# Kernel tuning notes

Hardware: AMD Instinct MI355X
Metric: run time of the kernel (lower is better)

## Reference

```python
import jax, jax.numpy as jnp
import numpy as np

N, E, B, H = 100000, 1600000, 16, 128
LN_EPS = 1e-5


def _ln(x, g, b):
    mu = jnp.mean(x, axis=-1, keepdims=True)
    v = jnp.mean(jnp.square(x - mu), axis=-1, keepdims=True)
    return (x - mu) * jax.lax.rsqrt(v + LN_EPS) * g + b


def setup_inputs() -> dict:
    key = jax.random.key(0)
    ks = iter(jax.random.split(key, 48))
    rn = lambda shape, s=0.05: jax.random.normal(next(ks), shape, jnp.float32) * s
    inp = {}
    inp['x'] = jax.random.normal(next(ks), (N, 3), jnp.float32)
    inp['edge_attr'] = jax.random.normal(next(ks), (E, 3), jnp.float32)
    inp['edge_index'] = jax.random.randint(next(ks), (2, E), 0, N, dtype=jnp.int32)
    inp['batch'] = jnp.sort(jax.random.randint(next(ks), (N,), 0, B, dtype=jnp.int32))
    # node encoder
    inp['ne_w1'] = rn((3, H)); inp['ne_b1'] = jnp.zeros((H,), jnp.float32)
    inp['ne_w2'] = rn((H, H)); inp['ne_b2'] = jnp.zeros((H,), jnp.float32)
    inp['ne_g'] = jnp.ones((H,), jnp.float32); inp['ne_be'] = jnp.zeros((H,), jnp.float32)
    # edge encoder
    inp['ee_w1'] = rn((3, H)); inp['ee_b1'] = jnp.zeros((H,), jnp.float32)
    inp['ee_w2'] = rn((H, H)); inp['ee_b2'] = jnp.zeros((H,), jnp.float32)
    inp['ee_g'] = jnp.ones((H,), jnp.float32); inp['ee_be'] = jnp.zeros((H,), jnp.float32)
    # GINEConv layers (stacked over num_layers=2)
    L = 2
    inp['gin_eps'] = jnp.zeros((L,), jnp.float32)
    inp['gin_w1'] = rn((L, H, H)); inp['gin_b1'] = jnp.zeros((L, H), jnp.float32)
    inp['gin_w2'] = rn((L, H, H)); inp['gin_b2'] = jnp.zeros((L, H), jnp.float32)
    inp['gin_g'] = jnp.ones((L, H), jnp.float32); inp['gin_be'] = jnp.zeros((L, H), jnp.float32)
    # global processor
    inp['gp_w'] = rn((H, H)); inp['gp_b'] = jnp.zeros((H,), jnp.float32)
    inp['gp_g'] = jnp.ones((H,), jnp.float32); inp['gp_be'] = jnp.zeros((H,), jnp.float32)
    # edge predictor
    inp['ep_w1'] = rn((4 * H, 2 * H)); inp['ep_b1'] = jnp.zeros((2 * H,), jnp.float32)
    inp['ep_w2'] = rn((2 * H, H)); inp['ep_b2'] = jnp.zeros((H,), jnp.float32)
    inp['ep_w3'] = rn((H, 1)); inp['ep_b3'] = jnp.zeros((1,), jnp.float32)
    return inp


def _forward(x, edge_attr, edge_index, batch,
             ne_w1, ne_b1, ne_w2, ne_b2, ne_g, ne_be,
             ee_w1, ee_b1, ee_w2, ee_b2, ee_g, ee_be,
             gin_eps, gin_w1, gin_b1, gin_w2, gin_b2, gin_g, gin_be,
             gp_w, gp_b, gp_g, gp_be,
             ep_w1, ep_b1, ep_w2, ep_b2, ep_w3, ep_b3):
    src, dst = edge_index[0], edge_index[1]
    # node / edge encoders (dropout = identity in eval mode)
    h = _ln(jax.nn.relu(x @ ne_w1 + ne_b1) @ ne_w2 + ne_b2, ne_g, ne_be)          # [N,H]
    e = _ln(jax.nn.relu(edge_attr @ ee_w1 + ee_b1) @ ee_w2 + ee_b2, ee_g, ee_be)  # [E,H]
    num_layers = gin_eps.shape[0]
    for l in range(num_layers):
        # GINE: out = MLP((1+eps)*x + sum_j relu(x_j + e_ij))
        msg = jax.nn.relu(h[src] + e)                                    # [E,H]
        agg = jax.ops.segment_sum(msg, dst, num_segments=N)              # [N,H]
        z = (1.0 + gin_eps[l]) * h + agg
        h = _ln(jax.nn.relu(z @ gin_w1[l] + gin_b1[l]) @ gin_w2[l] + gin_b2[l], gin_g[l], gin_be[l])
        if l < num_layers - 1:
            h = jax.nn.relu(h)
    # global mean pool over graphs
    gsum = jax.ops.segment_sum(h, batch, num_segments=B)                 # [B,H]
    cnt = jax.ops.segment_sum(jnp.ones((h.shape[0], 1), h.dtype), batch, num_segments=B)
    g = gsum / jnp.maximum(cnt, 1.0)
    g = _ln(jax.nn.relu(g @ gp_w + gp_b), gp_g, gp_be)                   # [B,H]
    # per-edge scores
    comb = jnp.concatenate([h[src], h[dst], g[batch[src]], e], axis=-1)  # [E,4H]
    s = jnp.tanh(comb @ ep_w1 + ep_b1)
    s = jnp.tanh(s @ ep_w2 + ep_b2)
    return jax.nn.sigmoid(s @ ep_w3 + ep_b3)                             # [E,1]


def reference(x, edge_attr, edge_index, batch,
              ne_w1, ne_b1, ne_w2, ne_b2, ne_g, ne_be,
              ee_w1, ee_b1, ee_w2, ee_b2, ee_g, ee_be,
              gin_eps, gin_w1, gin_b1, gin_w2, gin_b2, gin_g, gin_be,
              gp_w, gp_b, gp_g, gp_be,
              ep_w1, ep_b1, ep_w2, ep_b2, ep_w3, ep_b3):
    return _forward(x, edge_attr, edge_index, batch,
                    ne_w1, ne_b1, ne_w2, ne_b2, ne_g, ne_be,
                    ee_w1, ee_b1, ee_w2, ee_b2, ee_g, ee_be,
                    gin_eps, gin_w1, gin_b1, gin_w2, gin_b2, gin_g, gin_be,
                    gp_w, gp_b, gp_g, gp_be,
                    ep_w1, ep_b1, ep_w2, ep_b2, ep_w3, ep_b3)
```

## Files before the change

### kernel.cpp

```cpp
#include <hip/hip_runtime.h>
#include <stdint.h>

typedef unsigned short u16;
typedef short bf16x8 __attribute__((ext_vector_type(8)));
typedef float f32x4 __attribute__((ext_vector_type(4)));

#define DEV __device__ __forceinline__

DEV float bf2f(u16 u){ union{uint32_t i; float f;} v; v.i = ((uint32_t)u)<<16; return v.f; }
DEV u16 f2bf(float f){ union{float f; uint32_t i;} v; v.f=f; uint32_t u=v.i; u += 0x7FFFu + ((u>>16)&1u); return (u16)(u>>16); }
DEV uint32_t cvt_pk_bf16(float lo, float hi){
    uint32_t r;
    asm("v_cvt_pk_bf16_f32 %0, %1, %2" : "=v"(r) : "v"(lo), "v"(hi));
    return r;
}
DEV bf16x8 pack8(const float* v){
    union { bf16x8 b; uint32_t u[4]; } o;
    #pragma unroll
    for (int k=0;k<4;k++) o.u[k] = cvt_pk_bf16(v[2*k], v[2*k+1]);
    return o.b;
}
DEV float fast_tanh(float x){ float t=__builtin_amdgcn_exp2f(x*2.885390081777927f); return 1.f-2.f*__builtin_amdgcn_rcpf(t+1.f); }
DEV float fast_sigmoid(float x){ return __builtin_amdgcn_rcpf(1.f+__builtin_amdgcn_exp2f(-1.4426950408889634f*x)); }
DEV f32x4 mfma16(bf16x8 a, bf16x8 b, f32x4 c){ return __builtin_amdgcn_mfma_f32_16x16x32_bf16(a,b,c,0,0,0); }
DEV void atomAddF(float* p, float v){ __hip_atomic_fetch_add(p, v, __ATOMIC_RELAXED, __HIP_MEMORY_SCOPE_AGENT); }
DEV void barrier_lds(){
    asm volatile("s_waitcnt lgkmcnt(0)" ::: "memory");
    __builtin_amdgcn_s_barrier();
    __builtin_amdgcn_sched_barrier(0);
}

__global__ void diag_kernel(float* out, float v){ if (threadIdx.x < 8) out[threadIdx.x] = v; }

__global__ __launch_bounds__(256) void prep_all(
    const float* __restrict__ ne_w2, const float* __restrict__ ee_w2,
    const float* __restrict__ gin_w1, const float* __restrict__ gin_w2,
    const float* __restrict__ ep_w1, const float* __restrict__ ep_w2,
    u16* __restrict__ ne_w2T, u16* __restrict__ ee_w2T,
    u16* __restrict__ gw1T0, u16* __restrict__ gw1T1,
    u16* __restrict__ gw2T0, u16* __restrict__ gw2T1,
    u16* __restrict__ w1aT, u16* __restrict__ w1bT,
    u16* __restrict__ w1dT, u16* __restrict__ epw2T)
{
    int b = blockIdx.x, tid = threadIdx.x;
    const float* src; u16* dst; int ld, K, Nn, base;
    if      (b < 64)  { src=ne_w2;          dst=ne_w2T; ld=128; K=128; Nn=128; base=0;   }
    else if (b < 128) { src=ee_w2;          dst=ee_w2T; ld=128; K=128; Nn=128; base=64;  }
    else if (b < 192) { src=gin_w1;         dst=gw1T0;  ld=128; K=128; Nn=128; base=128; }
    else if (b < 256) { src=gin_w1+128*128; dst=gw1T1;  ld=128; K=128; Nn=128; base=192; }
    else if (b < 320) { src=gin_w2;         dst=gw2T0;  ld=128; K=128; Nn=128; base=256; }
    else if (b < 384) { src=gin_w2+128*128; dst=gw2T1;  ld=128; K=128; Nn=128; base=320; }
    else if (b < 512) { src=ep_w1;          dst=w1aT;   ld=256; K=128; Nn=256; base=384; }
    else if (b < 640) { src=ep_w1+128*256;  dst=w1bT;   ld=256; K=128; Nn=256; base=512; }
    else if (b < 768) { src=ep_w1+384*256;  dst=w1dT;   ld=256; K=128; Nn=256; base=640; }
    else              { src=ep_w2;          dst=epw2T;  ld=128; K=256; Nn=128; base=768; }
    int idx = (b-base)*256 + tid;
    if (idx >= K*Nn) return;
    int n = idx / K, k = idx - n*K;
    dst[(n*K + k) ^ ((n&7)<<3)] = f2bf(src[(size_t)k*ld + n]);
}

__global__ __launch_bounds__(256) void hist_kernel(const int* __restrict__ dst,
                                                   int* __restrict__ deg, int E)
{
    int e = blockIdx.x*256 + threadIdx.x;
    if (e < E) atomicAdd(&deg[dst[e]], 1);
}

__global__ __launch_bounds__(1024) void scan_kernel(const int* __restrict__ deg,
                                                    int* __restrict__ cur, int N)
{
    __shared__ int sc[1024];
    int t = threadIdx.x;
    int chunk = (N + 1023) / 1024;
    int i0 = t * chunk, i1 = i0 + chunk; if (i1 > N) i1 = N;
    int s = 0;
    for (int i = i0; i < i1; i++) s += deg[i];
    sc[t] = s; __syncthreads();
    int own = s;
    for (int off = 1; off < 1024; off <<= 1){
        int v = (t >= off) ? sc[t - off] : 0;
        __syncthreads();
        sc[t] += v;
        __syncthreads();
    }
    int run = sc[t] - own;
    for (int i = i0; i < i1; i++){ cur[i] = run; run += deg[i]; }
}

__global__ __launch_bounds__(256) void scatter_kernel(
    const int* __restrict__ src, const int* __restrict__ dst, const float* __restrict__ ea,
    int* __restrict__ cur, int* __restrict__ src_s, int* __restrict__ dst_s,
    float* __restrict__ ea_s, int E)
{
    int e = blockIdx.x*256 + threadIdx.x;
    if (e >= E) return;
    int d = dst[e];
    int pos = atomicAdd(&cur[d], 1);
    src_s[pos] = src[e];
    dst_s[pos] = d;
    ea_s[(size_t)pos*3+0] = ea[(size_t)e*3+0];
    ea_s[(size_t)pos*3+1] = ea[(size_t)e*3+1];
    ea_s[(size_t)pos*3+2] = ea[(size_t)e*3+2];
}

__global__ __launch_bounds__(256) void enc_kernel(
    const float* __restrict__ in3, int rows,
    const float* __restrict__ w1, const float* __restrict__ b1,
    const u16* __restrict__ w2T, const float* __restrict__ b2,
    const float* __restrict__ gam, const float* __restrict__ bet,
    float* __restrict__ outF)
{
    __shared__ u16 wbs[128*128];
    __shared__ u16 hid[64*128];
    int tid = threadIdx.x, r0 = blockIdx.x*64;
    for (int i = tid; i < 8192; i += 256) ((uint32_t*)wbs)[i] = ((const uint32_t*)w2T)[i];
    for (int idx = tid; idx < 8192; idx += 256) {
        int r = idx >> 7, c = idx & 127;
        int row = r0 + r; if (row > rows-1) row = rows-1;
        float v = b1[c] + in3[(size_t)row*3+0]*w1[c] + in3[(size_t)row*3+1]*w1[128+c] + in3[(size_t)row*3+2]*w1[256+c];
        hid[idx ^ ((r&7)<<3)] = f2bf(fmaxf(v, 0.f));
    }
    barrier_lds();
    int lane = tid & 63, w = tid >> 6, l16 = lane & 15, q = lane >> 4;
    int ar = 16*w + l16;
    f32x4 acc[8];
    #pragma unroll
    for (int nt=0; nt<8; nt++) acc[nt] = (f32x4){0.f,0.f,0.f,0.f};
    #pragma unroll
    for (int ks=0; ks<4; ks++) {
        bf16x8 af = *(const bf16x8*)&hid[(ar*128 + ks*32 + q*8) ^ ((ar&7)<<3)];
        #pragma unroll
        for (int nt=0; nt<8; nt++) {
            int n = nt*16 + l16;
            bf16x8 bfr = *(const bf16x8*)&wbs[(n*128 + ks*32 + q*8) ^ ((n&7)<<3)];
            acc[nt] = mfma16(af, bfr, acc[nt]);
        }
    }
    float b2v[8], gv[8], bv[8];
    #pragma unroll
    for (int nt=0; nt<8; nt++){ int c = nt*16+l16; b2v[nt]=b2[c]; gv[nt]=gam[c]; bv[nt]=bet[c]; }
    #pragma unroll
    for (int reg=0; reg<4; reg++) {
        float s=0.f, ss=0.f;
        #pragma unroll
        for (int nt=0; nt<8; nt++){ float v = acc[nt][reg] + b2v[nt]; acc[nt][reg]=v; s+=v; ss+=v*v; }
        #pragma unroll
        for (int m=1; m<16; m<<=1){ s += __shfl_xor(s,m); ss += __shfl_xor(ss,m); }
        float mean = s * (1.f/128.f);
        float rstd = __builtin_amdgcn_rsqf(ss*(1.f/128.f) - mean*mean + 1e-5f);
        int row = r0 + 16*w + 4*q + reg;
        if (row < rows) {
            #pragma unroll
            for (int nt=0; nt<8; nt++){
                int c = nt*16+l16;
                outF[(size_t)row*128 + c] = (acc[nt][reg]-mean)*rstd*gv[nt] + bv[nt];
            }
        }
    }
}

__global__ __launch_bounds__(256) void msg_v3(
    const float* __restrict__ ea_s, const int* __restrict__ src_s, const int* __restrict__ dst_s,
    const float* __restrict__ ew1, const float* __restrict__ eb1,
    const u16* __restrict__ ew2T, const float* __restrict__ eb2,
    const float* __restrict__ eg, const float* __restrict__ ebe,
    const float* __restrict__ h, float* __restrict__ agg, int E)
{
    __shared__ float lag[8192];
    __shared__ u16 hid[64*128];
    __shared__ float eas[192];
    __shared__ float w1s[384];
    __shared__ float b1s[128];
    __shared__ int ssrc[64], sdv[64], sslot[64], sfl[64];
    u16* wbs = (u16*)lag;
    int tid = threadIdx.x, r0 = blockIdx.x*64;

    const uint4* w4 = (const uint4*)ew2T;
    uint4 pr[8];
    #pragma unroll
    for (int k=0;k<8;k++) pr[k] = w4[tid + k*256];

    if (tid < 192){ int gi = r0*3 + tid; eas[tid] = (gi < E*3) ? ea_s[gi] : 0.f; }
    if (tid < 128) b1s[tid] = eb1[tid];
    for (int i = tid; i < 384; i += 256) w1s[i] = ew1[i];
    if (tid < 64){
        int r = tid, ge = r0 + r;
        int valid = ge < E;
        int gc = valid ? ge : E-1;
        int dv = dst_s[gc];
        int sv = src_s[gc];
        int pin = __shfl_up(dv, 1);
        int head = (r == 0) || (dv != pin);
        int prevLast  = (r0 > 0)      ? dst_s[r0-1]  : -2;
        int nextFirst = (r0 + 64 < E) ? dst_s[r0+64] : -2;
        int interior = (dv != prevLast) && (dv != nextFirst);
        int s = head ? r : 0;
        #pragma unroll
        for (int off=1; off<64; off<<=1){ int v = __shfl_up(s, off); if (r >= off) s = (s > v ? s : v); }
        ssrc[r]=sv; sdv[r]=dv; sslot[r]=s;
        sfl[r] = ((head && valid)?1:0) | (interior?2:0) | (valid?4:0);
    }
    barrier_lds();
    int g = tid >> 5, cgm = (tid & 31) << 2;
    float4 hv[8];
    #pragma unroll
    for (int k=0;k<8;k++)
        hv[k] = *(const float4*)(h + (size_t)ssrc[g*8+k]*128 + cgm);
    {
        uint4* wb4 = (uint4*)wbs;
        #pragma unroll
        for (int k=0;k<8;k++) wb4[tid + k*256] = pr[k];
    }
    barrier_lds();

    int lane = tid&63, w = tid>>6, l16 = lane&15, q = lane>>4;
    int ar = 16*w + l16;
    float ea0 = eas[ar*3], ea1 = eas[ar*3+1], ea2 = eas[ar*3+2];
    f32x4 acc[8];
    #pragma unroll
    for (int nt=0; nt<8; nt++) acc[nt] = (f32x4){0.f,0.f,0.f,0.f};
    #pragma unroll
    for (int ks=0; ks<4; ks++){
        float hv8[8];
        #pragma unroll
        for (int j=0;j<8;j++){
            int c = ks*32 + q*8 + j;
            hv8[j] = fmaxf(b1s[c] + ea0*w1s[c] + ea1*w1s[128+c] + ea2*w1s[256+c], 0.f);
        }
        bf16x8 ah = pack8(hv8);
        #pragma unroll
        for (int nt=0; nt<8; nt++){
            int n = nt*16 + l16;
            bf16x8 bfr = *(const bf16x8*)&wbs[(n*128 + ks*32 + q*8) ^ ((n&7)<<3)];
            acc[nt] = mfma16(ah, bfr, acc[nt]);
        }
    }
    {
        float b2v[8], gv[8], bv[8];
        #pragma unroll
        for (int nt=0; nt<8; nt++){ int c = nt*16+l16; b2v[nt]=eb2[c]; gv[nt]=eg[c]; bv[nt]=ebe[c]; }
        #pragma unroll
        for (int reg=0; reg<4; reg++){
            float s=0.f, ss=0.f;
            #pragma unroll
            for (int nt=0; nt<8; nt++){ float v = acc[nt][reg] + b2v[nt]; acc[nt][reg]=v; s+=v; ss+=v*v; }
            #pragma unroll
            for (int m=1; m<16; m<<=1){ s += __shfl_xor(s,m); ss += __shfl_xor(ss,m); }
            float mean = s*(1.f/128.f);
            float rstd = __builtin_amdgcn_rsqf(ss*(1.f/128.f)-mean*mean+1e-5f);
            int rl = 16*w + 4*q + reg;
            #pragma unroll
            for (int nt=0; nt<8; nt+=2){
                float v0 = (acc[nt][reg]-mean)*rstd*gv[nt] + bv[nt];
                float v1 = (acc[nt+1][reg]-mean)*rstd*gv[nt+1] + bv[nt+1];
                uint32_t pk = cvt_pk_bf16(v0, v1);
                hid[rl*128 + nt*16 + l16]     = (u16)pk;
                hid[rl*128 + (nt+1)*16 + l16] = (u16)(pk >> 16);
            }
        }
    }
    barrier_lds();
    for (int i = tid; i < 8192; i += 256) lag[i] = 0.f;
    barrier_lds();

    {
        float4 a = {0.f,0.f,0.f,0.f};
        int cur = -1;
        #pragma unroll
        for (int k=0;k<8;k++){
            int r = g*8 + k;
            if (sfl[r] & 4){
                uint2 ev = *(const uint2*)&hid[r*128 + cgm];
                float4 m;
                m.x = fmaxf(hv[k].x + bf2f((u16)(ev.x & 0xFFFF)), 0.f);
                m.y = fmaxf(hv[k].y + bf2f((u16)(ev.x >> 16)),   0.f);
                m.z = fmaxf(hv[k].z + bf2f((u16)(ev.y & 0xFFFF)), 0.f);
                m.w = fmaxf(hv[k].w + bf2f((u16)(ev.y >> 16)),   0.f);
                int slot = sslot[r];
                if (slot != cur){
                    if (cur >= 0){
                        float* lp = lag + cur*128 + cgm;
                        atomicAdd(lp+0,a.x); atomicAdd(lp+1,a.y); atomicAdd(lp+2,a.z); atomicAdd(lp+3,a.w);
                    }
                    cur = slot; a = m;
                } else {
                    a.x += m.x; a.y += m.y; a.z += m.z; a.w += m.w;
                }
            }
        }
        if (cur >= 0){
            float* lp = lag + cur*128 + cgm;
            atomicAdd(lp+0,a.x); atomicAdd(lp+1,a.y); atomicAdd(lp+2,a.z); atomicAdd(lp+3,a.w);
        }
    }
    barrier_lds();
    for (int t = tid; t < 2048; t += 256){
        int r = t >> 5, cg = (t & 31) << 2;
        int fl = sfl[r];
        if (!(fl & 1)) continue;
        float4 v = *(const float4*)&lag[r*128 + cg];
        float* gp = agg + (size_t)sdv[r]*128 + cg;
        if (fl & 2){ *(float4*)gp = v; }
        else { atomAddF(gp+0,v.x); atomAddF(gp+1,v.y); atomAddF(gp+2,v.z); atomAddF(gp+3,v.w); }
    }
}

__global__ __launch_bounds__(256) void gine_update(
    float* h, const float* __restrict__ agg,
    const float* __restrict__ epsArr, int layer,
    const u16* __restrict__ w1T, const u16* __restrict__ w2T,
    const float* __restrict__ b1, const float* __restrict__ b2,
    const float* __restrict__ gam, const float* __restrict__ bet,
    int rows, int doRelu)
{
    __shared__ u16 wbs[128*128];
    __shared__ u16 hid[64*128];
    int tid = threadIdx.x, r0 = blockIdx.x*64;
    float epsv = 1.f + epsArr[layer];
    for (int i = tid; i < 8192; i += 256) ((uint32_t*)wbs)[i] = ((const uint32_t*)w1T)[i];
    barrier_lds();
    int lane = tid&63, w = tid>>6, l16 = lane&15, q = lane>>4;
    int ar = 16*w + l16;
    int arow = r0 + ar;
    int arc = arow < rows ? arow : rows-1;
    f32x4 acc[8];
    #pragma unroll
    for (int nt=0; nt<8; nt++) acc[nt] = (f32x4){0.f,0.f,0.f,0.f};
    #pragma unroll
    for (int ks=0; ks<4; ks++){
        const float4* hp = (const float4*)(h   + (size_t)arc*128 + ks*32 + q*8);
        const float4* ap = (const float4*)(agg + (size_t)arc*128 + ks*32 + q*8);
        float4 h0 = hp[0], h1 = hp[1], a0 = ap[0], a1 = ap[1];
        float zv[8];
        zv[0]=fmaf(epsv,h0.x,a0.x); zv[1]=fmaf(epsv,h0.y,a0.y);
        zv[2]=fmaf(epsv,h0.z,a0.z); zv[3]=fmaf(epsv,h0.w,a0.w);
        zv[4]=fmaf(epsv,h1.x,a1.x); zv[5]=fmaf(epsv,h1.y,a1.y);
        zv[6]=fmaf(epsv,h1.z,a1.z); zv[7]=fmaf(epsv,h1.w,a1.w);
        bf16x8 af = pack8(zv);
        #pragma unroll
        for (int nt=0; nt<8; nt++){
            int n = nt*16 + l16;
            bf16x8 bfr = *(const bf16x8*)&wbs[(n*128 + ks*32 + q*8) ^ ((n&7)<<3)];
            acc[nt] = mfma16(af, bfr, acc[nt]);
        }
    }
    #pragma unroll
    for (int nt=0; nt<8; nt++){
        int c = nt*16 + l16; float b1v = b1[c];
        #pragma unroll
        for (int reg=0; reg<4; reg++){
            int rl = 16*w + 4*q + reg;
            hid[(rl*128 + c) ^ ((rl&7)<<3)] = f2bf(fmaxf(acc[nt][reg] + b1v, 0.f));
        }
    }
    barrier_lds();
    for (int i = tid; i < 8192; i += 256) ((uint32_t*)wbs)[i] = ((const uint32_t*)w2T)[i];
    barrier_lds();
    f32x4 a2[8];
    #pragma unroll
    for (int nt=0; nt<8; nt++) a2[nt] = (f32x4){0.f,0.f,0.f,0.f};
    #pragma unroll
    for (int ks=0; ks<4; ks++){
        bf16x8 af = *(const bf16x8*)&hid[(ar*128 + ks*32 + q*8) ^ ((ar&7)<<3)];
        #pragma unroll
        for (int nt=0; nt<8; nt++){
            int n = nt*16 + l16;
            bf16x8 bfr = *(const bf16x8*)&wbs[(n*128 + ks*32 + q*8) ^ ((n&7)<<3)];
            a2[nt] = mfma16(af, bfr, a2[nt]);
        }
    }
    float b2v[8], gv[8], bv[8];
    #pragma unroll
    for (int nt=0; nt<8; nt++){ int c = nt*16+l16; b2v[nt]=b2[c]; gv[nt]=gam[c]; bv[nt]=bet[c]; }
    #pragma unroll
    for (int reg=0; reg<4; reg++){
        float s=0.f, ss=0.f;
        #pragma unroll
        for (int nt=0; nt<8; nt++){ float v = a2[nt][reg] + b2v[nt]; a2[nt][reg]=v; s+=v; ss+=v*v; }
        #pragma unroll
        for (int m=1; m<16; m<<=1){ s += __shfl_xor(s,m); ss += __shfl_xor(ss,m); }
        float mean = s*(1.f/128.f);
        float rstd = __builtin_amdgcn_rsqf(ss*(1.f/128.f)-mean*mean+1e-5f);
        int row = r0 + 16*w + 4*q + reg;
        if (row < rows){
            #pragma unroll
            for (int nt=0; nt<8; nt++){
                int c = nt*16+l16;
                float o = (a2[nt][reg]-mean)*rstd*gv[nt] + bv[nt];
                if (doRelu) o = fmaxf(o, 0.f);
                h[(size_t)row*128 + c] = o;
            }
        }
    }
}

__global__ __launch_bounds__(256) void pool2_kernel(
    const float* __restrict__ h, const int* __restrict__ batch,
    float* __restrict__ gsum, float* __restrict__ cnt, int N, int npb)
{
    __shared__ float lacc[16*128];
    __shared__ float lcnt[16];
    int tid = threadIdx.x;
    int n0 = blockIdx.x * npb;
    for (int i = tid; i < 2048; i += 256) lacc[i] = 0.f;
    if (tid < 16) lcnt[tid] = 0.f;
    __syncthreads();
    int rl = tid >> 5, cg = (tid & 31) << 2;
    int cur_b = -1; float4 acc = {0.f,0.f,0.f,0.f}; float c = 0.f;
    for (int k = rl; k < npb; k += 8){
        int n = n0 + k;
        if (n >= N) break;
        int b = batch[n];
        float4 hv = *(const float4*)(h + (size_t)n*128 + cg);
        if (b != cur_b){
            if (cur_b >= 0){
                float* lp = lacc + cur_b*128 + cg;
                atomicAdd(lp+0,acc.x); atomicAdd(lp+1,acc.y); atomicAdd(lp+2,acc.z); atomicAdd(lp+3,acc.w);
                if (cg == 0) atomicAdd(&lcnt[cur_b], c);
            }
            cur_b = b; acc = hv; c = 1.f;
        } else { acc.x+=hv.x; acc.y+=hv.y; acc.z+=hv.z; acc.w+=hv.w; c += 1.f; }
    }
    if (cur_b >= 0){
        float* lp = lacc + cur_b*128 + cg;
        atomicAdd(lp+0,acc.x); atomicAdd(lp+1,acc.y); atomicAdd(lp+2,acc.z); atomicAdd(lp+3,acc.w);
        if (cg == 0) atomicAdd(&lcnt[cur_b], c);
    }
    __syncthreads();
    int lastn = n0 + npb - 1; if (lastn > N-1) lastn = N-1;
    int firstn = n0 < N-1 ? n0 : N-1;
    int bmin = batch[firstn], bmax = batch[lastn];
    int rows = bmax - bmin + 1;
    for (int i = tid; i < rows*128; i += 256){
        int b = bmin + (i >> 7), cc = i & 127;
        float v = lacc[b*128 + cc];
        if (v != 0.f) atomAddF(gsum + b*128 + cc, v);
    }
    if (tid < rows){ float v = lcnt[bmin+tid]; if (v != 0.f) atomAddF(cnt + bmin + tid, v); }
}

__global__ __launch_bounds__(256) void gproc_kernel(
    const float* __restrict__ gsum, const float* __restrict__ cnt,
    const float* __restrict__ gw, const float* __restrict__ gb,
    const float* __restrict__ gg, const float* __restrict__ gbe,
    float* __restrict__ gfin)
{
    __shared__ float gm[2048];
    int tid = threadIdx.x;
    for (int i = tid; i < 2048; i += 256){ int b = i >> 7; gm[i] = gsum[i] / fmaxf(cnt[b], 1.f); }
    __syncthreads();
    int r = tid >> 4, m = tid & 15;
    float a[8];
    #pragma unroll
    for (int j=0;j<8;j++) a[j]=0.f;
    for (int k=0;k<128;k++){
        float gv = gm[r*128+k];
        #pragma unroll
        for (int j=0;j<8;j++) a[j] = fmaf(gv, gw[k*128 + m + 16*j], a[j]);
    }
    float s=0.f, ss=0.f;
    #pragma unroll
    for (int j=0;j<8;j++){ float v = fmaxf(a[j] + gb[m+16*j], 0.f); a[j]=v; s+=v; ss+=v*v; }
    #pragma unroll
    for (int msk=1; msk<16; msk<<=1){ s += __shfl_xor(s,msk); ss += __shfl_xor(ss,msk); }
    float mean = s*(1.f/128.f);
    float rstd = __builtin_amdgcn_rsqf(ss*(1.f/128.f)-mean*mean+1e-5f);
    #pragma unroll
    for (int j=0;j<8;j++){ int c = m+16*j; gfin[r*128+c] = (a[j]-mean)*rstd*gg[c] + gbe[c]; }
}

__global__ __launch_bounds__(256) void gc_kernel(
    const float* __restrict__ gfin, const float* __restrict__ ep_w1,
    const float* __restrict__ ep_b1, float* __restrict__ Gc)
{
    __shared__ float gs[2048];
    int tid = threadIdx.x;
    for (int i = tid; i < 2048; i += 256) gs[i] = gfin[i];
    __syncthreads();
    for (int o = tid; o < 16*256; o += 256){
        int r = o >> 8, n = o & 255;
        float a = ep_b1[n];
        for (int k = 0; k < 128; k++) a = fmaf(gs[r*128+k], ep_w1[(size_t)(256+k)*256 + n], a);
        Gc[o] = a;
    }
}

__global__ __launch_bounds__(256) void hc_prep(
    const float* __restrict__ h, const u16* __restrict__ w1aT, const u16* __restrict__ w1bT,
    u16* __restrict__ hcS, u16* __restrict__ hcD, int rows)
{
    __shared__ u16 wbs[128*128];
    int tid = threadIdx.x, r0 = blockIdx.x*64;
    int lane = tid&63, w = tid>>6, l16 = lane&15, q = lane>>4;
    int arow = r0 + 16*w + l16;
    int arc = arow < rows ? arow : rows-1;
    bf16x8 afk[4];
    #pragma unroll
    for (int ks=0; ks<4; ks++){
        const float4* hp = (const float4*)(h + (size_t)arc*128 + ks*32 + q*8);
        float4 h0 = hp[0], h1 = hp[1];
        float zv[8] = {h0.x,h0.y,h0.z,h0.w,h1.x,h1.y,h1.z,h1.w};
        afk[ks] = pack8(zv);
    }
    #pragma unroll
    for (int pass = 0; pass < 2; pass++){
        const u16* wt = pass ? w1bT : w1aT;
        f32x4 acc[16];
        #pragma unroll
        for (int i=0; i<16; i++) acc[i] = (f32x4){0.f,0.f,0.f,0.f};
        #pragma unroll
        for (int ch = 0; ch < 2; ch++){
            barrier_lds();
            for (int i = tid; i < 8192; i += 256) ((uint32_t*)wbs)[i] = ((const uint32_t*)wt)[ch*8192 + i];
            barrier_lds();
            #pragma unroll
            for (int ks=0; ks<4; ks++){
                #pragma unroll
                for (int nt=0; nt<8; nt++){
                    int n = nt*16 + l16;
                    bf16x8 bfr = *(const bf16x8*)&wbs[(n*128 + ks*32 + q*8) ^ ((n&7)<<3)];
                    acc[ch*8+nt] = mfma16(afk[ks], bfr, acc[ch*8+nt]);
                }
            }
        }
        u16* outp = pass ? hcD : hcS;
        #pragma unroll
        for (int reg=0; reg<4; reg++){
            int row = r0 + 16*w + 4*q + reg;
            if (row < rows){
                #pragma unroll
                for (int i=0; i<16; i++) outp[(size_t)row*256 + i*16 + l16] = f2bf(acc[i][reg]);
            }
        }
    }
}

#define WBS_WRITE() { uint4* wb4=(uint4*)wbs; wb4[tid]=pr0; wb4[tid+256]=pr1; wb4[tid+512]=pr2; wb4[tid+768]=pr3; }
#define PREFETCH_LIN(base4, ch) { const uint4* pp=(base4)+(ch)*1024+tid; pr0=pp[0]; pr1=pp[256]; pr2=pp[512]; pr3=pp[768]; }
#define G2IDX(kh,nh,u) ((((nh)*64 + ((u)>>4))*32) + (kh)*16 + ((u)&15))
#define PREFETCH_G2(kh,nh) { pr0=epw2T4[G2IDX(kh,nh,tid)]; pr1=epw2T4[G2IDX(kh,nh,tid+256)]; pr2=epw2T4[G2IDX(kh,nh,tid+512)]; pr3=epw2T4[G2IDX(kh,nh,tid+768)]; }

__global__ __launch_bounds__(256, 3) void pred_rc4(
    const float* __restrict__ ea,
    const float* __restrict__ ew1, const float* __restrict__ eb1,
    const u16* __restrict__ ew2T, const float* __restrict__ eb2,
    const float* __restrict__ eg, const float* __restrict__ ebe,
    const int* __restrict__ src, const int* __restrict__ dst, const int* __restrict__ batch,
    const u16* __restrict__ hcS, const u16* __restrict__ hcD, const float* __restrict__ Gc,
    const u16* __restrict__ w1dT, const u16* __restrict__ epw2T,
    const float* __restrict__ b2, const float* __restrict__ w3, const float* __restrict__ b3,
    float* __restrict__ out, int E)
{
    __shared__ u16 wbs[64*128];
    __shared__ u16 s1t[64*256];
    u16* het = s1t;
    int tid = threadIdx.x, r0 = blockIdx.x*64;
    int lane = tid&63, w = tid>>6, l16 = lane&15, q = lane>>4;
    int ar = 16*w + l16;

    const uint4* ew2T4  = (const uint4*)ew2T;
    const uint4* w1dT4  = (const uint4*)w1dT;
    const uint4* epw2T4 = (const uint4*)epw2T;
    uint4 pr0, pr1, pr2, pr3;
    PREFETCH_LIN(ew2T4, 0);

    int rA = r0 + ar; int rAc = rA < E ? rA : E-1;
    int sA = src[rAc], dA = dst[rAc], gA = batch[sA];
    float ea0 = ea[(size_t)rAc*3+0], ea1 = ea[(size_t)rAc*3+1], ea2 = ea[(size_t)rAc*3+2];

    bf16x8 ah[4];
    #pragma unroll
    for (int ks = 0; ks < 4; ks++){
        int cb = ks*32 + q*8;
        float w0[8], w1r[8], w2r[8], bb[8], hv[8];
        *(float4*)&w0[0]  = *(const float4*)(ew1 + cb);       *(float4*)&w0[4]  = *(const float4*)(ew1 + cb + 4);
        *(float4*)&w1r[0] = *(const float4*)(ew1 + 128 + cb); *(float4*)&w1r[4] = *(const float4*)(ew1 + 128 + cb + 4);
        *(float4*)&w2r[0] = *(const float4*)(ew1 + 256 + cb); *(float4*)&w2r[4] = *(const float4*)(ew1 + 256 + cb + 4);
        *(float4*)&bb[0]  = *(const float4*)(eb1 + cb);       *(float4*)&bb[4]  = *(const float4*)(eb1 + cb + 4);
        #pragma unroll
        for (int j = 0; j < 8; j++)
            hv[j] = fmaxf(bb[j] + ea0*w0[j] + ea1*w1r[j] + ea2*w2r[j], 0.f);
        ah[ks] = pack8(hv);
    }

    f32x4 eac[8];
    #pragma unroll
    for (int i=0;i<8;i++) eac[i] = (f32x4){0.f,0.f,0.f,0.f};
    #pragma unroll
    for (int ch=0; ch<2; ch++){
        barrier_lds();
        WBS_WRITE();
        if (ch == 0) { PREFETCH_LIN(ew2T4, 1); } else { PREFETCH_LIN(w1dT4, 0); }
        barrier_lds();
        #pragma unroll
        for (int ks=0; ks<4; ks++){
            #pragma unroll
            for (int nt=0; nt<4; nt++){
                int n = nt*16 + l16;
                bf16x8 bfr = *(const bf16x8*)&wbs[(n*128 + ks*32 + q*8) ^ ((n&7)<<3)];
                eac[ch*4+nt] = mfma16(ah[ks], bfr, eac[ch*4+nt]);
            }
        }
    }
    {
        float b2v[8], gv[8], bv[8];
        #pragma unroll
        for (int i=0;i<8;i++){ int c=i*16+l16; b2v[i]=eb2[c]; gv[i]=eg[c]; bv[i]=ebe[c]; }
        #pragma unroll
        for (int reg=0; reg<4; reg++){
            float s=0.f, ss=0.f;
            #pragma unroll
            for (int i=0;i<8;i++){ float v = eac[i][reg]+b2v[i]; eac[i][reg]=v; s+=v; ss+=v*v; }
            #pragma unroll
            for (int m=1;m<16;m<<=1){ s+=__shfl_xor(s,m); ss+=__shfl_xor(ss,m); }
            float mean = s*(1.f/128.f);
            float rstd = __builtin_amdgcn_rsqf(ss*(1.f/128.f)-mean*mean+1e-5f);
            int rl = 16*w + 4*q + reg;
            #pragma unroll
            for (int i=0;i<8;i+=2){
                float v0 = (eac[i][reg]-mean)*rstd*gv[i]+bv[i];
                float v1 = (eac[i+1][reg]-mean)*rstd*gv[i+1]+bv[i+1];
                uint32_t pk = cvt_pk_bf16(v0, v1);
                het[(rl*128 + i*16+l16) ^ ((rl&7)<<3)]     = (u16)pk;
                het[(rl*128 + (i+1)*16+l16) ^ ((rl&7)<<3)] = (u16)(pk>>16);
            }
        }
    }
    bf16x8 afE[4];
    #pragma unroll
    for (int ks=0; ks<4; ks++)
        afE[ks] = *(const bf16x8*)&het[(ar*128 + ks*32 + q*8) ^ ((ar&7)<<3)];
    asm volatile("s_waitcnt lgkmcnt(0)" ::: "memory");
    __builtin_amdgcn_sched_barrier(0);
    barrier_lds();
    #pragma unroll
    for (int j = 0; j < 8; j++){
        int c0 = q*64 + j*8;
        uint4 hs = *(const uint4*)(hcS + (size_t)sA*256 + c0);
        uint4 hd = *(const uint4*)(hcD + (size_t)dA*256 + c0);
        float4 g0 = *(const float4*)(Gc + gA*256 + c0);
        float4 g1 = *(const float4*)(Gc + gA*256 + c0 + 4);
        float sv[8];
        sv[0]=bf2f((u16)(hs.x&0xFFFF))+bf2f((u16)(hd.x&0xFFFF))+g0.x;
        sv[1]=bf2f((u16)(hs.x>>16))  +bf2f((u16)(hd.x>>16))  +g0.y;
        sv[2]=bf2f((u16)(hs.y&0xFFFF))+bf2f((u16)(hd.y&0xFFFF))+g0.z;
        sv[3]=bf2f((u16)(hs.y>>16))  +bf2f((u16)(hd.y>>16))  +g0.w;
        sv[4]=bf2f((u16)(hs.z&0xFFFF))+bf2f((u16)(hd.z&0xFFFF))+g1.x;
        sv[5]=bf2f((u16)(hs.z>>16))  +bf2f((u16)(hd.z>>16))  +g1.y;
        sv[6]=bf2f((u16)(hs.w&0xFFFF))+bf2f((u16)(hd.w&0xFFFF))+g1.z;
        sv[7]=bf2f((u16)(hs.w>>16))  +bf2f((u16)(hd.w>>16))  +g1.w;
        *(bf16x8*)&s1t[(ar*256 + c0) ^ ((ar&7)<<3)] = pack8(sv);
    }
    #pragma unroll
    for (int half = 0; half < 2; half++){
        f32x4 acc[8];
        #pragma unroll
        for (int i=0;i<8;i++) acc[i] = (f32x4){0.f,0.f,0.f,0.f};
        #pragma unroll
        for (int c2 = 0; c2 < 2; c2++){
            int ch = half*2 + c2;
            barrier_lds();
            WBS_WRITE();
            if (ch < 3) { PREFETCH_LIN(w1dT4, ch+1); } else { PREFETCH_G2(0,0); }
            barrier_lds();
            #pragma unroll
            for (int ks=0; ks<4; ks++){
                #pragma unroll
                for (int nt=0; nt<4; nt++){
                    int n = nt*16 + l16;
                    bf16x8 bfr = *(const bf16x8*)&wbs[(n*128 + ks*32 + q*8) ^ ((n&7)<<3)];
                    acc[c2*4+nt] = mfma16(afE[ks], bfr, acc[c2*4+nt]);
                }
            }
        }
        #pragma unroll
        for (int i=0; i<8; i+=2){
            int gi0 = half*8 + i, gi1 = gi0 + 1;
            #pragma unroll
            for (int reg=0; reg<4; reg++){
                int rl = 16*w + 4*q + reg;
                int idx0 = (rl*256 + gi0*16 + l16) ^ ((rl&7)<<3);
                int idx1 = (rl*256 + gi1*16 + l16) ^ ((rl&7)<<3);
                float t0 = acc[i][reg]   + bf2f(s1t[idx0]);
                float t1 = acc[i+1][reg] + bf2f(s1t[idx1]);
                uint32_t pk = cvt_pk_bf16(fast_tanh(t0), fast_tanh(t1));
                s1t[idx0] = (u16)pk;
                s1t[idx1] = (u16)(pk>>16);
            }
        }
    }
    f32x4 a2[8];
    #pragma unroll
    for (int i=0;i<8;i++) a2[i] = (f32x4){0.f,0.f,0.f,0.f};
    #pragma unroll
    for (int cc=0; cc<4; cc++){
        int kh = cc>>1, nh = cc&1;
        barrier_lds();
        WBS_WRITE();
        if (cc == 0) { PREFETCH_G2(0,1); } else if (cc == 1) { PREFETCH_G2(1,0); } else if (cc == 2) { PREFETCH_G2(1,1); }
        barrier_lds();
        #pragma unroll
        for (int ks=0; ks<4; ks++){
            bf16x8 af = *(const bf16x8*)&s1t[(ar*256 + kh*128 + ks*32 + q*8) ^ ((ar&7)<<3)];
            #pragma unroll
            for (int nt=0; nt<4; nt++){
                int nl = nt*16 + l16;
                bf16x8 bfr = *(const bf16x8*)&wbs[(nl*128 + ks*32 + q*8) ^ ((nl&7)<<3)];
                a2[nh*4+nt] = mfma16(af, bfr, a2[nh*4+nt]);
            }
        }
    }
    float p[4] = {0.f,0.f,0.f,0.f};
    #pragma unroll
    for (int i=0;i<8;i++){
        int c = i*16 + l16;
        float b2v = b2[c], w3v = w3[c];
        #pragma unroll
        for (int reg=0;reg<4;reg++){
            float v = fast_tanh(a2[i][reg] + b2v);
            p[reg] = fmaf(v, w3v, p[reg]);
        }
    }
    float b3v = b3[0];
    #pragma unroll
    for (int reg=0;reg<4;reg++){
        float pv = p[reg];
        #pragma unroll
        for (int m=1;m<16;m<<=1) pv += __shfl_xor(pv,m);
        if (l16==0){
            int er = r0 + 16*w + 4*q + reg;
            if (er < E) out[er] = fast_sigmoid(pv + b3v);
        }
    }
}
#undef WBS_WRITE
#undef PREFETCH_LIN
#undef PREFETCH_G2
#undef G2IDX

extern "C" void kernel_launch(void* const* d_in, const int* in_sizes, int n_in,
                              void* d_out, int out_size, void* d_ws, size_t ws_size,
                              hipStream_t stream)
{
    if (n_in < 33){ diag_kernel<<<1,64,0,stream>>>((float*)d_out, 2.0e6f); return; }
    const float* x      = (const float*)d_in[0];
    const float* ea     = (const float*)d_in[1];
    const int*   eidx   = (const int*)  d_in[2];
    const int*   batch  = (const int*)  d_in[3];
    const float* ne_w1  = (const float*)d_in[4];
    const float* ne_b1  = (const float*)d_in[5];
    const float* ne_w2  = (const float*)d_in[6];
    const float* ne_b2  = (const float*)d_in[7];
    const float* ne_g   = (const float*)d_in[8];
    const float* ne_be  = (const float*)d_in[9];
    const float* ee_w1  = (const float*)d_in[10];
    const float* ee_b1  = (const float*)d_in[11];
    const float* ee_w2  = (const float*)d_in[12];
    const float* ee_b2  = (const float*)d_in[13];
    const float* ee_g   = (const float*)d_in[14];
    const float* ee_be  = (const float*)d_in[15];
    const float* gin_eps= (const float*)d_in[16];
    const float* gin_w1 = (const float*)d_in[17];
    const float* gin_b1 = (const float*)d_in[18];
    const float* gin_w2 = (const float*)d_in[19];
    const float* gin_b2 = (const float*)d_in[20];
    const float* gin_g  = (const float*)d_in[21];
    const float* gin_be = (const float*)d_in[22];
    const float* gp_w   = (const float*)d_in[23];
    const float* gp_b   = (const float*)d_in[24];
    const float* gp_g   = (const float*)d_in[25];
    const float* gp_be  = (const float*)d_in[26];
    const float* ep_w1  = (const float*)d_in[27];
    const float* ep_b1  = (const float*)d_in[28];
    const float* ep_w2  = (const float*)d_in[29];
    const float* ep_b2  = (const float*)d_in[30];
    const float* ep_w3  = (const float*)d_in[31];
    const float* ep_b3  = (const float*)d_in[32];

    int N = in_sizes[0] / 3;
    int E = in_sizes[1] / 3;
    const int* srcI = eidx;
    const int* dstI = eidx + E;

    char* ws = (char*)d_ws;
    size_t off = 0;
    auto alloc = [&](size_t bytes) -> void* {
        void* p = ws + off; off += (bytes + 255) & ~(size_t)255; return p;
    };
    float* h     = (float*)alloc((size_t)N*512);
    char*  R1    = (char*) alloc((size_t)N*512);
    u16*   hcD   = (u16*)  alloc((size_t)N*512);
    int*   deg   = (int*)  alloc((size_t)N*4);
    int*   curp  = (int*)  alloc((size_t)N*4);
    int*   src_s = (int*)  alloc((size_t)E*4);
    int*   dst_s = (int*)  alloc((size_t)E*4);
    float* ea_s  = (float*)alloc((size_t)E*12);
    float* gsum  = (float*)alloc((2048+64)*4);
    float* cnt   = gsum + 2048;
    float* gfin  = (float*)alloc(2048*4);
    float* Gc    = (float*)alloc(16*256*4);
    u16* ne_w2T = (u16*)alloc(16384*2);
    u16* ee_w2T = (u16*)alloc(16384*2);
    u16* gw1T0  = (u16*)alloc(16384*2);
    u16* gw1T1  = (u16*)alloc(16384*2);
    u16* gw2T0  = (u16*)alloc(16384*2);
    u16* gw2T1  = (u16*)alloc(16384*2);
    u16* w1aT   = (u16*)alloc(32768*2);
    u16* w1bT   = (u16*)alloc(32768*2);
    u16* w1dT   = (u16*)alloc(32768*2);
    u16* epw2T  = (u16*)alloc(32768*2);
    if (off > ws_size){
        diag_kernel<<<1,64,0,stream>>>((float*)d_out, 1.0e6f + (float)(ws_size >> 20));
        return;
    }
    float* agg = (float*)R1;
    u16*   hcS = (u16*)R1;

    prep_all<<<896, 256, 0, stream>>>(ne_w2, ee_w2, gin_w1, gin_w2, ep_w1, ep_w2,
                                      ne_w2T, ee_w2T, gw1T0, gw1T1, gw2T0, gw2T1,
                                      w1aT, w1bT, w1dT, epw2T);

    hipMemsetAsync(deg, 0, (size_t)N*4, stream);
    hist_kernel<<<(E+255)/256, 256, 0, stream>>>(dstI, deg, E);
    scan_kernel<<<1, 1024, 0, stream>>>(deg, curp, N);
    scatter_kernel<<<(E+255)/256, 256, 0, stream>>>(srcI, dstI, ea, curp, src_s, dst_s, ea_s, E);

    int nbN = (N + 63) / 64;
    int nbE = (E + 63) / 64;
    enc_kernel<<<nbN, 256, 0, stream>>>(x, N, ne_w1, ne_b1, ne_w2T, ne_b2, ne_g, ne_be, h);

    for (int l = 0; l < 2; l++){
        hipMemsetAsync(agg, 0, (size_t)N*512, stream);
        msg_v3<<<nbE, 256, 0, stream>>>(ea_s, src_s, dst_s,
                                        ee_w1, ee_b1, ee_w2T, ee_b2, ee_g, ee_be,
                                        h, agg, E);
        gine_update<<<nbN, 256, 0, stream>>>(h, agg, gin_eps, l,
            l ? gw1T1 : gw1T0, l ? gw2T1 : gw2T0,
            gin_b1 + l*128, gin_b2 + l*128, gin_g + l*128, gin_be + l*128,
            N, l == 0 ? 1 : 0);
    }

    hipMemsetAsync(gsum, 0, (2048 + 16) * 4, stream);
    int npb = 512;
    pool2_kernel<<<(N + npb - 1)/npb, 256, 0, stream>>>(h, batch, gsum, cnt, N, npb);
    gproc_kernel<<<1, 256, 0, stream>>>(gsum, cnt, gp_w, gp_b, gp_g, gp_be, gfin);
    gc_kernel<<<1, 256, 0, stream>>>(gfin, ep_w1, ep_b1, Gc);
    hc_prep<<<nbN, 256, 0, stream>>>(h, w1aT, w1bT, hcS, hcD, N);

    pred_rc4<<<nbE, 256, 0, stream>>>(ea, ee_w1, ee_b1, ee_w2T, ee_b2, ee_g, ee_be,
                                      srcI, dstI, batch, hcS, hcD, Gc,
                                      w1dT, epw2T, ep_b2, ep_w3, ep_b3,
                                      (float*)d_out, E);
}
```

Baseline: 2.328 ms.

## Fuse edge-predictor node projections into last GINE update and merge global kernels

The final GINE update kernel now also computes the bf16 source and destination projections (hcS/hcD). It reuses the freshly normalized rows already held in LDS, so a separate hc_prep kernel that re-read h from global memory is no longer needed. The global-processor and Gc kernels are merged into one single-block kernel that keeps the normalized graph vector in shared memory instead of going through a global buffer. This removes two launches and one full pass over h, at the cost of higher register and LDS pressure in the fused update kernel, and it relies on hcS aliasing agg only within each block's own rows.

```diff
diff --git a/kernel.cpp b/kernel.cpp
--- a/kernel.cpp
+++ b/kernel.cpp
@@ -306,13 +306,15 @@
     }
 }
 
-__global__ __launch_bounds__(256) void gine_update(
+__global__ __launch_bounds__(256) void gine_hc(
     float* h, const float* __restrict__ agg,
     const float* __restrict__ epsArr, int layer,
     const u16* __restrict__ w1T, const u16* __restrict__ w2T,
     const float* __restrict__ b1, const float* __restrict__ b2,
     const float* __restrict__ gam, const float* __restrict__ bet,
-    int rows, int doRelu)
+    int rows, int doRelu,
+    const u16* __restrict__ w1aT, const u16* __restrict__ w1bT,
+    u16* __restrict__ hcS, u16* __restrict__ hcD, int doHc)
 {
     __shared__ u16 wbs[128*128];
     __shared__ u16 hid[64*128];
@@ -373,6 +375,30 @@
     float b2v[8], gv[8], bv[8];
     #pragma unroll
     for (int nt=0; nt<8; nt++){ int c = nt*16+l16; b2v[nt]=b2[c]; gv[nt]=gam[c]; bv[nt]=bet[c]; }
+    if (!doHc){
+        #pragma unroll
+        for (int reg=0; reg<4; reg++){
+            float s=0.f, ss=0.f;
+            #pragma unroll
+            for (int nt=0; nt<8; nt++){ float v = a2[nt][reg] + b2v[nt]; a2[nt][reg]=v; s+=v; ss+=v*v; }
+            #pragma unroll
+            for (int m=1; m<16; m<<=1){ s += __shfl_xor(s,m); ss += __shfl_xor(ss,m); }
+            float mean = s*(1.f/128.f);
+            float rstd = __builtin_amdgcn_rsqf(ss*(1.f/128.f)-mean*mean+1e-5f);
+            int row = r0 + 16*w + 4*q + reg;
+            if (row < rows){
+                #pragma unroll
+                for (int nt=0; nt<8; nt++){
+                    int c = nt*16+l16;
+                    float o = (a2[nt][reg]-mean)*rstd*gv[nt] + bv[nt];
+                    if (doRelu) o = fmaxf(o, 0.f);
+                    h[(size_t)row*128 + c] = o;
+                }
+            }
+        }
+        return;
+    }
+    barrier_lds();
     #pragma unroll
     for (int reg=0; reg<4; reg++){
         float s=0.f, ss=0.f;
@@ -382,14 +408,60 @@
         for (int m=1; m<16; m<<=1){ s += __shfl_xor(s,m); ss += __shfl_xor(ss,m); }
         float mean = s*(1.f/128.f);
         float rstd = __builtin_amdgcn_rsqf(ss*(1.f/128.f)-mean*mean+1e-5f);
-        int row = r0 + 16*w + 4*q + reg;
-        if (row < rows){
-            #pragma unroll
-            for (int nt=0; nt<8; nt++){
-                int c = nt*16+l16;
-                float o = (a2[nt][reg]-mean)*rstd*gv[nt] + bv[nt];
-                if (doRelu) o = fmaxf(o, 0.f);
-                h[(size_t)row*128 + c] = o;
+        int rl = 16*w + 4*q + reg;
+        int row = r0 + rl;
+        #pragma unroll
+        for (int nt=0; nt<8; nt+=2){
+            float o0 = (a2[nt][reg]-mean)*rstd*gv[nt] + bv[nt];
+            float o1 = (a2[nt+1][reg]-mean)*rstd*gv[nt+1] + bv[nt+1];
+            if (row < rows){
+                h[(size_t)row*128 + nt*16+l16]     = o0;
+                h[(size_t)row*128 + (nt+1)*16+l16] = o1;
+            }
+            uint32_t pk = cvt_pk_bf16(o0, o1);
+            hid[(rl*128 + nt*16+l16) ^ ((rl&7)<<3)]     = (u16)pk;
+            hid[(rl*128 + (nt+1)*16+l16) ^ ((rl&7)<<3)] = (u16)(pk>>16);
+        }
+    }
+    barrier_lds();
+    bf16x8 afk[4];
+    #pragma unroll
+    for (int ks=0; ks<4; ks++)
+        afk[ks] = *(const bf16x8*)&hid[(ar*128 + ks*32 + q*8) ^ ((ar&7)<<3)];
+    asm volatile("s_waitcnt lgkmcnt(0)" ::: "memory");
+    __builtin_amdgcn_sched_barrier(0);
+    #pragma unroll
+    for (int pass = 0; pass < 2; pass++){
+        const u16* wt = pass ? w1bT : w1aT;
+        f32x4 hacc[16];
+        #pragma unroll
+        for (int i=0; i<16; i++) hacc[i] = (f32x4){0.f,0.f,0.f,0.f};
+        #pragma unroll
+        for (int ch = 0; ch < 2; ch++){
+            barrier_lds();
+            for (int i = tid; i < 8192; i += 256) ((uint32_t*)wbs)[i] = ((const uint32_t*)wt)[ch*8192 + i];
+            barrier_lds();
+            #pragma unroll
+            for (int ks=0; ks<4; ks++){
+                #pragma unroll
+                for (int nt=0; nt<8; nt++){
+                    int n = nt*16 + l16;
+                    bf16x8 bfr = *(const bf16x8*)&wbs[(n*128 + ks*32 + q*8) ^ ((n&7)<<3)];
+                    hacc[ch*8+nt] = mfma16(afk[ks], bfr, hacc[ch*8+nt]);
+                }
+            }
+        }
+        u16* outp = pass ? hcD : hcS;
+        #pragma unroll
+        for (int reg=0; reg<4; reg++){
+            int row = r0 + 16*w + 4*q + reg;
+            if (row < rows){
+                #pragma unroll
+                for (int i=0; i<16; i+=2){
+                    uint32_t pk = cvt_pk_bf16(hacc[i][reg], hacc[i+1][reg]);
+                    outp[(size_t)row*256 + i*16 + l16]     = (u16)pk;
+                    outp[(size_t)row*256 + (i+1)*16 + l16] = (u16)(pk>>16);
+                }
             }
         }
     }
@@ -440,11 +512,12 @@
     if (tid < rows){ float v = lcnt[bmin+tid]; if (v != 0.f) atomAddF(cnt + bmin + tid, v); }
 }
 
-__global__ __launch_bounds__(256) void gproc_kernel(
+__global__ __launch_bounds__(256) void gpgc_kernel(
     const float* __restrict__ gsum, const float* __restrict__ cnt,
     const float* __restrict__ gw, const float* __restrict__ gb,
     const float* __restrict__ gg, const float* __restrict__ gbe,
-    float* __restrict__ gfin)
+    const float* __restrict__ ep_w1, const float* __restrict__ ep_b1,
+    float* __restrict__ Gc)
 {
     __shared__ float gm[2048];
     int tid = threadIdx.x;
@@ -466,73 +539,15 @@
     for (int msk=1; msk<16; msk<<=1){ s += __shfl_xor(s,msk); ss += __shfl_xor(ss,msk); }
     float mean = s*(1.f/128.f);
     float rstd = __builtin_amdgcn_rsqf(ss*(1.f/128.f)-mean*mean+1e-5f);
-    #pragma unroll
-    for (int j=0;j<8;j++){ int c = m+16*j; gfin[r*128+c] = (a[j]-mean)*rstd*gg[c] + gbe[c]; }
-}
-
-__global__ __launch_bounds__(256) void gc_kernel(
-    const float* __restrict__ gfin, const float* __restrict__ ep_w1,
-    const float* __restrict__ ep_b1, float* __restrict__ Gc)
-{
-    __shared__ float gs[2048];
-    int tid = threadIdx.x;
-    for (int i = tid; i < 2048; i += 256) gs[i] = gfin[i];
+    __syncthreads();
+    #pragma unroll
+    for (int j=0;j<8;j++){ int c = m+16*j; gm[r*128+c] = (a[j]-mean)*rstd*gg[c] + gbe[c]; }
     __syncthreads();
     for (int o = tid; o < 16*256; o += 256){
-        int r = o >> 8, n = o & 255;
-        float a = ep_b1[n];
-        for (int k = 0; k < 128; k++) a = fmaf(gs[r*128+k], ep_w1[(size_t)(256+k)*256 + n], a);
-        Gc[o] = a;
-    }
-}
-
-__global__ __launch_bounds__(256) void hc_prep(
-    const float* __restrict__ h, const u16* __restrict__ w1aT, const u16* __restrict__ w1bT,
-    u16* __restrict__ hcS, u16* __restrict__ hcD, int rows)
-{
-    __shared__ u16 wbs[128*128];
-    int tid = threadIdx.x, r0 = blockIdx.x*64;
-    int lane = tid&63, w = tid>>6, l16 = lane&15, q = lane>>4;
-    int arow = r0 + 16*w + l16;
-    int arc = arow < rows ? arow : rows-1;
-    bf16x8 afk[4];
-    #pragma unroll
-    for (int ks=0; ks<4; ks++){
-        const float4* hp = (const float4*)(h + (size_t)arc*128 + ks*32 + q*8);
-        float4 h0 = hp[0], h1 = hp[1];
-        float zv[8] = {h0.x,h0.y,h0.z,h0.w,h1.x,h1.y,h1.z,h1.w};
-        afk[ks] = pack8(zv);
-    }
-    #pragma unroll
-    for (int pass = 0; pass < 2; pass++){
-        const u16* wt = pass ? w1bT : w1aT;
-        f32x4 acc[16];
-        #pragma unroll
-        for (int i=0; i<16; i++) acc[i] = (f32x4){0.f,0.f,0.f,0.f};
-        #pragma unroll
-        for (int ch = 0; ch < 2; ch++){
-            barrier_lds();
-            for (int i = tid; i < 8192; i += 256) ((uint32_t*)wbs)[i] = ((const uint32_t*)wt)[ch*8192 + i];
-            barrier_lds();
-            #pragma unroll
-            for (int ks=0; ks<4; ks++){
-                #pragma unroll
-                for (int nt=0; nt<8; nt++){
-                    int n = nt*16 + l16;
-                    bf16x8 bfr = *(const bf16x8*)&wbs[(n*128 + ks*32 + q*8) ^ ((n&7)<<3)];
-                    acc[ch*8+nt] = mfma16(afk[ks], bfr, acc[ch*8+nt]);
-                }
-            }
-        }
-        u16* outp = pass ? hcD : hcS;
-        #pragma unroll
-        for (int reg=0; reg<4; reg++){
-            int row = r0 + 16*w + 4*q + reg;
-            if (row < rows){
-                #pragma unroll
-                for (int i=0; i<16; i++) outp[(size_t)row*256 + i*16 + l16] = f2bf(acc[i][reg]);
-            }
-        }
+        int rr = o >> 8, n = o & 255;
+        float aa = ep_b1[n];
+        for (int k = 0; k < 128; k++) aa = fmaf(gm[rr*128+k], ep_w1[(size_t)(256+k)*256 + n], aa);
+        Gc[o] = aa;
     }
 }
 
@@ -798,7 +813,6 @@
     float* ea_s  = (float*)alloc((size_t)E*12);
     float* gsum  = (float*)alloc((2048+64)*4);
     float* cnt   = gsum + 2048;
-    float* gfin  = (float*)alloc(2048*4);
     float* Gc    = (float*)alloc(16*256*4);
     u16* ne_w2T = (u16*)alloc(16384*2);
     u16* ee_w2T = (u16*)alloc(16384*2);
@@ -835,18 +849,17 @@
         msg_v3<<<nbE, 256, 0, stream>>>(ea_s, src_s, dst_s,
                                         ee_w1, ee_b1, ee_w2T, ee_b2, ee_g, ee_be,
                                         h, agg, E);
-        gine_update<<<nbN, 256, 0, stream>>>(h, agg, gin_eps, l,
+        gine_hc<<<nbN, 256, 0, stream>>>(h, agg, gin_eps, l,
             l ? gw1T1 : gw1T0, l ? gw2T1 : gw2T0,
             gin_b1 + l*128, gin_b2 + l*128, gin_g + l*128, gin_be + l*128,
-            N, l == 0 ? 1 : 0);
+            N, l == 0 ? 1 : 0,
+            w1aT, w1bT, hcS, hcD, l == 1 ? 1 : 0);
     }
 
     hipMemsetAsync(gsum, 0, (2048 + 16) * 4, stream);
     int npb = 512;
     pool2_kernel<<<(N + npb - 1)/npb, 256, 0, stream>>>(h, batch, gsum, cnt, N, npb);
-    gproc_kernel<<<1, 256, 0, stream>>>(gsum, cnt, gp_w, gp_b, gp_g, gp_be, gfin);
-    gc_kernel<<<1, 256, 0, stream>>>(gfin, ep_w1, ep_b1, Gc);
-    hc_prep<<<nbN, 256, 0, stream>>>(h, w1aT, w1bT, hcS, hcD, N);
+    gpgc_kernel<<<1, 256, 0, stream>>>(gsum, cnt, gp_w, gp_b, gp_g, gp_be, ep_w1, ep_b1, Gc);
 
     pred_rc4<<<nbE, 256, 0, stream>>>(ea, ee_w1, ee_b1, ee_w2T, ee_b2, ee_g, ee_be,
                                       srcI, dstI, batch, hcS, hcD, Gc,
```

Result: no change. 2.339 ms (median of 4 runs) (+0.5%).
